# Optimization experiments

Hardware: AMD Instinct MI355X
Metric: run time of the kernel (lower is better)

Reference implementation:

```python
import jax, jax.numpy as jnp
import numpy as np

N_NODES = 50000
N_EDGES = 800000
C_IN = 64
C_OUT = 64
K = 3


def setup_inputs() -> dict:
    key = jax.random.key(0)
    k1, k2, k3, k4, k5, k6 = jax.random.split(key, 6)
    x = jax.random.normal(k1, (N_NODES, C_IN), dtype=jnp.float32)
    edge_index = jax.random.randint(k2, (2, N_EDGES), 0, N_NODES, dtype=jnp.int32)
    edge_weight = jax.random.uniform(k3, (N_EDGES,), dtype=jnp.float32)
    # Xavier-uniform init for [K, C_IN, C_OUT] (fan over last two dims)
    limit = float(np.sqrt(6.0 / (C_IN + C_OUT)))
    theta_forward = jax.random.uniform(k4, (K, C_IN, C_OUT), minval=-limit, maxval=limit, dtype=jnp.float32)
    theta_backward = jax.random.uniform(k5, (K, C_IN, C_OUT), minval=-limit, maxval=limit, dtype=jnp.float32)
    return {
        "x": x,
        "edge_index": edge_index,
        "edge_weight": edge_weight,
        "theta_forward": theta_forward,
        "theta_backward": theta_backward,
    }


def _propagate(x, row, col, edge_weight, n_nodes):
    # degree normalization: deg[i] = sum of edge_weight over edges with row == i
    deg = jax.ops.segment_sum(edge_weight, row, num_segments=n_nodes)
    deg_inv = jnp.where(deg > 0, jax.lax.rsqrt(jnp.where(deg > 0, deg, 1.0)), 0.0)
    norm = deg_inv[row] * edge_weight * deg_inv[col]      # [E]
    msg = norm[:, None] * x[col]                          # [E, C] gather-scale
    return jax.ops.segment_sum(msg, row, num_segments=n_nodes)  # scatter-add -> [N, C]


def reference(x, edge_index, edge_weight, theta_forward, theta_backward):
    row, col = edge_index[0], edge_index[1]
    n_nodes = x.shape[0]
    k = theta_forward.shape[0]
    Tx_0 = x
    Tx_1 = _propagate(x, row, col, edge_weight, n_nodes)
    out = Tx_0 @ theta_forward[0] + Tx_1 @ theta_backward[0]
    for i in range(1, k):
        Tx_2 = _propagate(Tx_1, row, col, edge_weight, n_nodes)
        out = out + Tx_2 @ theta_forward[i] + Tx_1 @ theta_backward[i]
        Tx_1 = Tx_2
    return out
```

## Files before the change

### kernel.cpp

```cpp
#include <hip/hip_runtime.h>
#include <hip/hip_fp16.h>


#define N_NODES 50000
#define N_EDGES 800000
#define C 64
#define CAP 64
#define NPART 196
#define CAPP 4608
#define EPB 8192
#define NEB 98
#define XH_BLOCKS 782
#define CW_BLOCKS 16

typedef _Float16 half8 __attribute__((ext_vector_type(8)));
typedef float f32x4 __attribute__((ext_vector_type(4)));

__global__ __launch_bounds__(1024) void scatter2_kernel(
        const int* __restrict__ row, const int* __restrict__ col,
        const float* __restrict__ w, int* __restrict__ percur,
        uint2* __restrict__ pedges,
        const float* __restrict__ x, __half* __restrict__ xh,
        const float* __restrict__ tf, const float* __restrict__ tb,
        _Float16* __restrict__ whc) {
    const int tid = threadIdx.x;
    if (blockIdx.x >= NEB + XH_BLOCKS) {
        int idx = (blockIdx.x - NEB - XH_BLOCKS) * 1024 + tid;
        int j = idx >> 12;
        int rem = idx & 4095;
        int ci = rem >> 6;
        int co = rem & 63;
        float v;
        if (j == 0)      v = tf[rem];
        else if (j == 1) v = tb[rem] + tb[4096 + rem];
        else if (j == 2) v = tf[4096 + rem] + tb[8192 + rem];
        else             v = tf[8192 + rem];
        whc[(j << 12) + (co << 6) + ci] = (_Float16)v;
        return;
    }
    if (blockIdx.x >= NEB) {
        int i = (blockIdx.x - NEB) * 1024 + tid;
        if (i < N_NODES * C / 4) {
            float4 v = ((const float4*)x)[i];
            union { float2 f2; __half2 h2[2]; } u;
            u.h2[0] = __floats2half2_rn(v.x, v.y);
            u.h2[1] = __floats2half2_rn(v.z, v.w);
            ((float2*)xh)[i] = u.f2;
        }
        return;
    }
    __shared__ int h[NPART];
    __shared__ int cur[NPART];
    uint2 ent[8];
    int pp[8];
    if (tid < NPART) h[tid] = 0;
    __syncthreads();
    int base = blockIdx.x * EPB;
#pragma unroll
    for (int i = 0; i < 8; ++i) {
        int e = base + i * 1024 + tid;
        pp[i] = -1;
        if (e < N_EDGES) {
            int r = row[e];
            unsigned int c = (unsigned int)col[e];
            unsigned int wh = (unsigned int)__half_as_ushort(__float2half_rn(w[e]));
            ent[i] = make_uint2((c << 16) | wh, (unsigned int)(r & 255));
            pp[i] = r >> 8;
            atomicAdd(&h[pp[i]], 1);
        }
    }
    __syncthreads();
    if (tid < NPART) cur[tid] = atomicAdd(&percur[tid], h[tid]);
    __syncthreads();
#pragma unroll
    for (int i = 0; i < 8; ++i) {
        if (pp[i] >= 0) {
            int slot = atomicAdd(&cur[pp[i]], 1);
            pedges[(size_t)pp[i] * CAPP + slot] = ent[i];
        }
    }
}

__global__ __launch_bounds__(1024) void build_kernel(
        const uint2* __restrict__ pedges, const int* __restrict__ percur,
        unsigned int* __restrict__ bkt, int* __restrict__ cnt,
        float* __restrict__ dinv) {
    __shared__ unsigned int lbuck[256 * CAP];
    __shared__ int lcnt[256];
    const int tid = threadIdx.x;
    const int p = blockIdx.x;
    if (tid < 256) lcnt[tid] = 0;
    __syncthreads();
    int e = min(percur[p], CAPP);
    const uint2* src = pedges + (size_t)p * CAPP;
    for (int i = tid; i < e; i += 1024) {
        uint2 en = src[i];
        int rl = (int)en.y;
        int slot = atomicAdd(&lcnt[rl], 1);
        if (slot < CAP) lbuck[(rl << 6) + slot] = en.x;
    }
    __syncthreads();
    if (tid < 256) {
        int m = min(lcnt[tid], CAP);
        int g = (p << 8) + tid;
        float sum = 0.f;
        for (int j = 0; j < m; ++j)
            sum += __half2float(__ushort_as_half(
                (unsigned short)(lbuck[(tid << 6) + j] & 0xFFFFu)));
        if (g < N_NODES) {
            cnt[g] = m;
            dinv[g] = (sum > 0.f) ? rsqrtf(sum) : 0.f;
        }
    }
    __syncthreads();
    const uint4* s4 = (const uint4*)lbuck;
    uint4* dst = (uint4*)(bkt + ((size_t)p << 14));
    for (int i = tid; i < 256 * CAP / 4; i += 1024) dst[i] = s4[i];
}

__global__ __launch_bounds__(256) void prop_kernel(
        const __half* __restrict__ xin, __half* __restrict__ xout,
        const int* __restrict__ cnt, const unsigned int* __restrict__ bkt,
        const float* __restrict__ dinv) {
    int wave = (blockIdx.x * blockDim.x + threadIdx.x) >> 6;
    int lane = threadIdx.x & 63;
    int q = lane >> 4;
    int ql = lane & 15;
    int node = (wave << 2) + q;
    if (node >= N_NODES) return;
    int m = min(cnt[node], CAP);
    int base = node << 6;
    float ax = 0.f, ay = 0.f, az = 0.f, aw = 0.f;
    for (int cb = 0; cb < m; cb += 16) {
        int cj = 0;
        float nj = 0.f;
        int idx = cb + ql;
        if (idx < m) {
            unsigned int b = bkt[base + idx];
            int c = (int)(b >> 16);
            cj = c << 6;
            nj = __half2float(__ushort_as_half((unsigned short)(b & 0xFFFFu))) * dinv[c];
        }
        int rem = m - cb;
        if (rem > 16) rem = 16;
        int mm = (rem + 7) & ~7;
        for (int jo = 0; jo < mm; jo += 8) {
            int cs[8];
            float ns[8];
            float2 vs[8];
#pragma unroll
            for (int t = 0; t < 8; ++t) {
                cs[t] = __shfl(cj, (q << 4) + jo + t);
                ns[t] = __shfl(nj, (q << 4) + jo + t);
            }
#pragma unroll
            for (int t = 0; t < 8; ++t)
                vs[t] = *(const float2*)(xin + cs[t] + (ql << 2));
#pragma unroll
            for (int t = 0; t < 8; ++t) {
                const __half2* hp = (const __half2*)&vs[t];
                float2 a = __half22float2(hp[0]);
                float2 b = __half22float2(hp[1]);
                ax += ns[t] * a.x;
                ay += ns[t] * a.y;
                az += ns[t] * b.x;
                aw += ns[t] * b.y;
            }
        }
    }
    float dr = dinv[node];
    union { float2 f2; __half2 h2[2]; } u;
    u.h2[0] = __floats2half2_rn(dr * ax, dr * ay);
    u.h2[1] = __floats2half2_rn(dr * az, dr * aw);
    *(float2*)(xout + base + (ql << 2)) = u.f2;
}

__global__ __launch_bounds__(256) void gemm_mfma_kernel(
        const __half* __restrict__ x0, const __half* __restrict__ x1,
        const __half* __restrict__ x2, const __half* __restrict__ x3,
        const _Float16* __restrict__ whc, float* __restrict__ out) {
    const int tid = threadIdx.x;
    const int wv = tid >> 6;
    const int lane = tid & 63;
    const int quad = lane >> 4;
    const int l16 = lane & 15;
    const int mbase = (blockIdx.x << 6) + (wv << 4);
    const __half* srcs[4] = {x0, x1, x2, x3};
    f32x4 acc0 = {}, acc1 = {}, acc2 = {}, acc3 = {};
    const int arow = mbase + l16;
    const bool aok = arow < N_NODES;
    const size_t abase = ((size_t)arow << 6) + (quad << 3);
    const half8 zero8 = {};
#pragma unroll
    for (int j = 0; j < 4; ++j) {
        const __half* src = srcs[j];
#pragma unroll
        for (int kk = 0; kk < 64; kk += 32) {
            half8 af = aok ? *(const half8*)(const void*)(src + abase + kk) : zero8;
            const _Float16* wb = whc + (j << 12) + kk + (quad << 3);
            half8 b0 = *(const half8*)(const void*)(wb + ((0 * 16 + l16) << 6));
            half8 b1 = *(const half8*)(const void*)(wb + ((1 * 16 + l16) << 6));
            half8 b2 = *(const half8*)(const void*)(wb + ((2 * 16 + l16) << 6));
            half8 b3 = *(const half8*)(const void*)(wb + ((3 * 16 + l16) << 6));
            acc0 = __builtin_amdgcn_mfma_f32_16x16x32_f16(af, b0, acc0, 0, 0, 0);
            acc1 = __builtin_amdgcn_mfma_f32_16x16x32_f16(af, b1, acc1, 0, 0, 0);
            acc2 = __builtin_amdgcn_mfma_f32_16x16x32_f16(af, b2, acc2, 0, 0, 0);
            acc3 = __builtin_amdgcn_mfma_f32_16x16x32_f16(af, b3, acc3, 0, 0, 0);
        }
    }
#pragma unroll
    for (int i = 0; i < 4; ++i) {
        int r = mbase + (quad << 2) + i;
        if (r < N_NODES) {
            float* dst = out + ((size_t)r << 6) + l16;
            dst[0]  = acc0[i];
            dst[16] = acc1[i];
            dst[32] = acc2[i];
            dst[48] = acc3[i];
        }
    }
}

extern "C" void kernel_launch(void* const* d_in, const int* in_sizes, int n_in,
                              void* d_out, int out_size, void* d_ws, size_t ws_size,
                              hipStream_t stream) {
    const float* x  = (const float*)d_in[0];
    const int*   ei = (const int*)d_in[1];
    const float* ew = (const float*)d_in[2];
    const float* tf = (const float*)d_in[3];
    const float* tb = (const float*)d_in[4];
    float* out = (float*)d_out;

    const int* row = ei;
    const int* col = ei + N_EDGES;

    const int NROWS_PAD = NPART * 256;
    float* ws = (float*)d_ws;
    size_t off = 0;
    int*    percur = (int*)(ws + off); off += 256;
    uint2*  pedges = (uint2*)(ws + off); off += (size_t)NPART * CAPP * 2;
    unsigned int* bkt = (unsigned int*)(ws + off); off += (size_t)NROWS_PAD * CAP;
    int*    cnt  = (int*)(ws + off); off += NROWS_PAD;
    float*  dinv = ws + off; off += NROWS_PAD;
    __half* xh   = (__half*)(ws + off); off += (size_t)N_NODES * C / 2;
    __half* tA   = (__half*)(ws + off); off += (size_t)N_NODES * C / 2;
    __half* tB   = (__half*)(ws + off); off += (size_t)N_NODES * C / 2;
    __half* tC   = (__half*)(ws + off); off += (size_t)N_NODES * C / 2;
    _Float16* whc = (_Float16*)(ws + off); off += 4 * 64 * 64 / 2;

    hipMemsetAsync(percur, 0, NPART * sizeof(int), stream);

    scatter2_kernel<<<NEB + XH_BLOCKS + CW_BLOCKS, 1024, 0, stream>>>(
        row, col, ew, percur, pedges, x, xh, tf, tb, whc);
    build_kernel<<<NPART, 1024, 0, stream>>>(pedges, percur, bkt, cnt, dinv);

    const int PB = (N_NODES + 15) / 16;
    prop_kernel<<<PB, 256, 0, stream>>>(xh, tA, cnt, bkt, dinv);
    prop_kernel<<<PB, 256, 0, stream>>>(tA, tB, cnt, bkt, dinv);
    prop_kernel<<<PB, 256, 0, stream>>>(tB, tC, cnt, bkt, dinv);

    const int GB = (N_NODES + 63) / 64;
    gemm_mfma_kernel<<<GB, 256, 0, stream>>>(xh, tA, tB, tC, whc, out);
}
```

Before: 165.9 us.

## Sort per-row neighbor lists by column and process in four column bands

The build kernel now insertion-sorts each row's neighbor bucket by source column and records the band boundaries (columns below 16K, 32K and 48K) packed with the count into one word. The propagation kernel processes each row's neighbors band by band, so concurrently running waves tend to gather from nearby regions of the feature array, which is meant to improve cache locality. This adds a serial sort per row in the build kernel and splits each row into up to four short spans. Those spans can leave more partially filled 8-wide groups, which wastes lanes and adds loop overhead.

```diff
diff --git a/kernel.cpp b/kernel.cpp
--- a/kernel.cpp
+++ b/kernel.cpp
@@ -83,7 +83,7 @@
 
 __global__ __launch_bounds__(1024) void build_kernel(
         const uint2* __restrict__ pedges, const int* __restrict__ percur,
-        unsigned int* __restrict__ bkt, int* __restrict__ cnt,
+        unsigned int* __restrict__ bkt, unsigned int* __restrict__ cpk,
         float* __restrict__ dinv) {
     __shared__ unsigned int lbuck[256 * CAP];
     __shared__ int lcnt[256];
@@ -102,13 +102,29 @@
     __syncthreads();
     if (tid < 256) {
         int m = min(lcnt[tid], CAP);
+        unsigned int* rowp = &lbuck[tid << 6];
+        for (int i = 1; i < m; ++i) {
+            unsigned int key = rowp[i];
+            int j = i - 1;
+            while (j >= 0 && (rowp[j] >> 16) > (key >> 16)) {
+                rowp[j + 1] = rowp[j];
+                --j;
+            }
+            rowp[j + 1] = key;
+        }
+        int o1 = 0, o2 = 0, o3 = 0;
+        float sum = 0.f;
+        for (int j = 0; j < m; ++j) {
+            unsigned int c = rowp[j] >> 16;
+            o1 += (c < 16384u);
+            o2 += (c < 32768u);
+            o3 += (c < 49152u);
+            sum += __half2float(__ushort_as_half((unsigned short)(rowp[j] & 0xFFFFu)));
+        }
         int g = (p << 8) + tid;
-        float sum = 0.f;
-        for (int j = 0; j < m; ++j)
-            sum += __half2float(__ushort_as_half(
-                (unsigned short)(lbuck[(tid << 6) + j] & 0xFFFFu)));
         if (g < N_NODES) {
-            cnt[g] = m;
+            cpk[g] = (unsigned int)o1 | ((unsigned int)o2 << 8) |
+                     ((unsigned int)o3 << 16) | ((unsigned int)m << 24);
             dinv[g] = (sum > 0.f) ? rsqrtf(sum) : 0.f;
         }
     }
@@ -118,30 +134,21 @@
     for (int i = tid; i < 256 * CAP / 4; i += 1024) dst[i] = s4[i];
 }
 
-__global__ __launch_bounds__(256) void prop_kernel(
-        const __half* __restrict__ xin, __half* __restrict__ xout,
-        const int* __restrict__ cnt, const unsigned int* __restrict__ bkt,
-        const float* __restrict__ dinv) {
-    int wave = (blockIdx.x * blockDim.x + threadIdx.x) >> 6;
-    int lane = threadIdx.x & 63;
-    int q = lane >> 4;
-    int ql = lane & 15;
-    int node = (wave << 2) + q;
-    if (node >= N_NODES) return;
-    int m = min(cnt[node], CAP);
-    int base = node << 6;
-    float ax = 0.f, ay = 0.f, az = 0.f, aw = 0.f;
-    for (int cb = 0; cb < m; cb += 16) {
+__device__ __forceinline__ void prop_span(
+        const __half* __restrict__ xin, const unsigned int* __restrict__ bktrow,
+        const float* __restrict__ dinv, int q, int ql, int s, int e2,
+        float& ax, float& ay, float& az, float& aw) {
+    for (int cb = s; cb < e2; cb += 16) {
         int cj = 0;
         float nj = 0.f;
         int idx = cb + ql;
-        if (idx < m) {
-            unsigned int b = bkt[base + idx];
+        if (idx < e2) {
+            unsigned int b = bktrow[idx];
             int c = (int)(b >> 16);
             cj = c << 6;
             nj = __half2float(__ushort_as_half((unsigned short)(b & 0xFFFFu))) * dinv[c];
         }
-        int rem = m - cb;
+        int rem = e2 - cb;
         if (rem > 16) rem = 16;
         int mm = (rem + 7) & ~7;
         for (int jo = 0; jo < mm; jo += 8) {
@@ -168,11 +175,34 @@
             }
         }
     }
+}
+
+__global__ __launch_bounds__(256) void prop_kernel(
+        const __half* __restrict__ xin, __half* __restrict__ xout,
+        const unsigned int* __restrict__ cpk, const unsigned int* __restrict__ bkt,
+        const float* __restrict__ dinv) {
+    int wave = (blockIdx.x * blockDim.x + threadIdx.x) >> 6;
+    int lane = threadIdx.x & 63;
+    int q = lane >> 4;
+    int ql = lane & 15;
+    int node = (wave << 2) + q;
+    if (node >= N_NODES) return;
+    unsigned int po = cpk[node];
+    int b1 = (int)(po & 255u);
+    int b2 = (int)((po >> 8) & 255u);
+    int b3 = (int)((po >> 16) & 255u);
+    int b4 = (int)(po >> 24);
+    const unsigned int* bktrow = bkt + ((size_t)node << 6);
+    float ax = 0.f, ay = 0.f, az = 0.f, aw = 0.f;
+    prop_span(xin, bktrow, dinv, q, ql, 0,  b1, ax, ay, az, aw);
+    prop_span(xin, bktrow, dinv, q, ql, b1, b2, ax, ay, az, aw);
+    prop_span(xin, bktrow, dinv, q, ql, b2, b3, ax, ay, az, aw);
+    prop_span(xin, bktrow, dinv, q, ql, b3, b4, ax, ay, az, aw);
     float dr = dinv[node];
     union { float2 f2; __half2 h2[2]; } u;
     u.h2[0] = __floats2half2_rn(dr * ax, dr * ay);
     u.h2[1] = __floats2half2_rn(dr * az, dr * aw);
-    *(float2*)(xout + base + (ql << 2)) = u.f2;
+    *(float2*)(xout + ((size_t)node << 6) + (ql << 2)) = u.f2;
 }
 
 __global__ __launch_bounds__(256) void gemm_mfma_kernel(
@@ -240,7 +270,7 @@
     int*    percur = (int*)(ws + off); off += 256;
     uint2*  pedges = (uint2*)(ws + off); off += (size_t)NPART * CAPP * 2;
     unsigned int* bkt = (unsigned int*)(ws + off); off += (size_t)NROWS_PAD * CAP;
-    int*    cnt  = (int*)(ws + off); off += NROWS_PAD;
+    unsigned int* cpk = (unsigned int*)(ws + off); off += NROWS_PAD;
     float*  dinv = ws + off; off += NROWS_PAD;
     __half* xh   = (__half*)(ws + off); off += (size_t)N_NODES * C / 2;
     __half* tA   = (__half*)(ws + off); off += (size_t)N_NODES * C / 2;
@@ -252,12 +282,12 @@
 
     scatter2_kernel<<<NEB + XH_BLOCKS + CW_BLOCKS, 1024, 0, stream>>>(
         row, col, ew, percur, pedges, x, xh, tf, tb, whc);
-    build_kernel<<<NPART, 1024, 0, stream>>>(pedges, percur, bkt, cnt, dinv);
+    build_kernel<<<NPART, 1024, 0, stream>>>(pedges, percur, bkt, cpk, dinv);
 
     const int PB = (N_NODES + 15) / 16;
-    prop_kernel<<<PB, 256, 0, stream>>>(xh, tA, cnt, bkt, dinv);
-    prop_kernel<<<PB, 256, 0, stream>>>(tA, tB, cnt, bkt, dinv);
-    prop_kernel<<<PB, 256, 0, stream>>>(tB, tC, cnt, bkt, dinv);
+    prop_kernel<<<PB, 256, 0, stream>>>(xh, tA, cpk, bkt, dinv);
+    prop_kernel<<<PB, 256, 0, stream>>>(tA, tB, cpk, bkt, dinv);
+    prop_kernel<<<PB, 256, 0, stream>>>(tB, tC, cpk, bkt, dinv);
 
     const int GB = (N_NODES + 63) / 64;
     gemm_mfma_kernel<<<GB, 256, 0, stream>>>(xh, tA, tB, tC, whc, out);
```

Measured after the change: 226.0 us. 36.2% more time.
